# Kernel tuning notes

Hardware: AMD Instinct MI355X
Metric: run time of the kernel (lower is better)

## Reference

```python
import jax, jax.numpy as jnp
import numpy as np

L, B, N, D, H, DH, DFF = 12, 4, 512, 768, 12, 64, 3072
SCALE = 1.0 / np.sqrt(DH).astype(np.float32)


def _ln(x, s, b):
    m = x.mean(-1, keepdims=True)
    v = ((x - m) ** 2).mean(-1, keepdims=True)
    return (x - m) * jax.lax.rsqrt(v + 1e-5) * s + b


def setup_inputs() -> dict:
    key = jax.random.key(0)
    ks = jax.random.split(key, 6)
    w = 0.02
    return {
        "x": jax.random.normal(ks[0], (B, N, D), jnp.float32),
        "ln1_s": jnp.ones((L, D), jnp.float32),
        "ln1_b": jnp.zeros((L, D), jnp.float32),
        "wqkv": jax.random.normal(ks[1], (L, D, 3 * H * DH), jnp.float32) * w,
        "wo": jax.random.normal(ks[2], (L, H * DH, D), jnp.float32) * w,
        "bo": jnp.zeros((L, D), jnp.float32),
        "ln2_s": jnp.ones((L, D), jnp.float32),
        "ln2_b": jnp.zeros((L, D), jnp.float32),
        "w1": jax.random.normal(ks[3], (L, D, DFF), jnp.float32) * w,
        "b1": jnp.zeros((L, DFF), jnp.float32),
        "w2": jax.random.normal(ks[4], (L, DFF, D), jnp.float32) * w,
        "b2": jnp.zeros((L, D), jnp.float32),
    }


def reference(x, ln1_s, ln1_b, wqkv, wo, bo, ln2_s, ln2_b, w1, b1, w2, b2):
    b, n, d = x.shape

    def layer(x, p):
        l1s, l1b, qkv_w, wo_, bo_, l2s, l2b, w1_, b1_, w2_, b2_ = p
        # --- pre-norm multi-head self-attention (softmax) ---
        h = _ln(x, l1s, l1b)
        qkv = h @ qkv_w                              # [b, n, 3*H*DH]
        q, k, v = jnp.split(qkv, 3, axis=-1)
        def heads(t):                                # [b, n, H*DH] -> [b, H, n, DH]
            return t.reshape(b, n, H, DH).transpose(0, 2, 1, 3)
        q, k, v = heads(q), heads(k), heads(v)
        scores = jnp.einsum("bhnd,bhmd->bhnm", q, k) * SCALE
        attn = jax.nn.softmax(scores, axis=-1)       # [b, H, n, n]
        o = jnp.einsum("bhnm,bhmd->bhnd", attn, v)
        o = o.transpose(0, 2, 1, 3).reshape(b, n, H * DH)
        x = x + (o @ wo_ + bo_)                      # residual 1 (dropout p=0)
        # --- pre-norm feed-forward (GELU, exact erf as in torch) ---
        h2 = _ln(x, l2s, l2b)
        ff = jax.nn.gelu(h2 @ w1_ + b1_, approximate=False) @ w2_ + b2_
        x = x + ff                                   # residual 2
        return x, attn

    out, weights = jax.lax.scan(
        layer, x, (ln1_s, ln1_b, wqkv, wo, bo, ln2_s, ln2_b, w1, b1, w2, b2)
    )
    return out, weights  # weights: [L, b, H, n, n], matching the per-layer list
```

## Files before the change

kernel.cpp:

```cpp
#include <hip/hip_runtime.h>
#include <hip/hip_bf16.h>

typedef __hip_bfloat16 bf16;
typedef float f32x4 __attribute__((ext_vector_type(4)));
typedef __bf16 b16x8 __attribute__((ext_vector_type(8)));

constexpr int Lc = 12, Bc = 4, Nc = 512, Dc = 768, Hc = 12, DHc = 64, DFFc = 3072;
constexpr int QKVc = 3 * Dc;
constexpr int Mrows = Bc * Nc;
constexpr float SCALE = 0.125f;

__device__ __forceinline__ bf16 f2b(float x) { return __float2bfloat16(x); }

__device__ __forceinline__ void mfma_bf16(f32x4& d, b16x8 a, b16x8 b) {
  d = __builtin_amdgcn_mfma_f32_16x16x32_bf16(a, b, d, 0, 0, 0);
}

__device__ __forceinline__ void gload16(const bf16* g, bf16* l) {
  __builtin_amdgcn_global_load_lds(
      (const __attribute__((address_space(1))) void*)g,
      (__attribute__((address_space(3))) void*)l, 16, 0, 0);
}

template <int BM, int BN, int WM, int WN, int MODE, int SPLITK = 1>
__global__ __launch_bounds__(256) void gemm_bt(
    const bf16* __restrict__ Abase, const bf16* __restrict__ Btbase,
    const float* __restrict__ bias, float* __restrict__ xres,
    bf16* __restrict__ outb_,
    int M, int N, int K, int lda, int ldb, int ldc) {
  constexpr int MI = WM / 16, NI = WN / 16;
  constexpr int NWN = BN / WN;
  const int tid = threadIdx.x;
  const int lane = tid & 63, wave = tid >> 6;
  const int wm = (wave / NWN) * WM, wn = (wave % NWN) * WN;
  const int tm0 = blockIdx.x * BM, tn0 = blockIdx.y * BN;
  const int z = blockIdx.z;

  const bf16* A = Abase;
  const bf16* Bt = Btbase;
  bf16* outb = outb_;

  if (MODE == 4) {
    A = Abase + (size_t)z * Nc * Nc;
    Bt = Btbase + (size_t)z * DHc * Nc;
    outb = outb_ + (size_t)(z / Hc) * Nc * Dc + (size_t)(z % Hc) * DHc;
  }

  const int Kslice = K / SPLITK;
  const int kbase = (SPLITK > 1) ? z * Kslice : 0;

  __shared__ __align__(16) bf16 As[2][BM * 32];
  __shared__ __align__(16) bf16 Bs[2][BN * 32];

  f32x4 acc[MI][NI] = {};

  const int nt = Kslice >> 5;

  auto stage = [&](int buf, int k0) {
    #pragma unroll
    for (int rr = 0; rr < BM / 64; rr++) {
      int e = rr * 2048 + tid * 8;
      int r = e >> 5, kk = e & 31;
      gload16(A + (size_t)(tm0 + r) * lda + (kbase + k0 + kk), &As[buf][e]);
    }
    #pragma unroll
    for (int rr = 0; rr < BN / 64; rr++) {
      int e = rr * 2048 + tid * 8;
      int r = e >> 5, kk = e & 31;
      gload16(Bt + (size_t)(tn0 + r) * ldb + (kbase + k0 + kk), &Bs[buf][e]);
    }
  };

  stage(0, 0);
  __syncthreads();

  int cur = 0;
  for (int kt = 0; kt < nt; kt++) {
    if (kt + 1 < nt) stage(cur ^ 1, (kt + 1) * 32);

    b16x8 af[MI], bfr[NI];
    #pragma unroll
    for (int i = 0; i < MI; i++)
      af[i] = *(const b16x8*)(&As[cur][(wm + i * 16 + (lane & 15)) * 32 + (lane >> 4) * 8]);
    #pragma unroll
    for (int j = 0; j < NI; j++)
      bfr[j] = *(const b16x8*)(&Bs[cur][(wn + j * 16 + (lane & 15)) * 32 + (lane >> 4) * 8]);
    #pragma unroll
    for (int i = 0; i < MI; i++)
      #pragma unroll
      for (int j = 0; j < NI; j++)
        mfma_bf16(acc[i][j], af[i], bfr[j]);

    __syncthreads();
    cur ^= 1;
  }

  const int r0 = (lane >> 4) * 4;
  const int c0 = lane & 15;
  #pragma unroll
  for (int i = 0; i < MI; i++) {
    #pragma unroll
    for (int j = 0; j < NI; j++) {
      #pragma unroll
      for (int r = 0; r < 4; r++) {
        int row = tm0 + wm + i * 16 + r0 + r;
        int col = tn0 + wn + j * 16 + c0;
        float v = acc[i][j][r];
        if (MODE == 0) {
          outb[(size_t)row * ldc + col] = f2b(v);
        } else if (MODE == 1) {
          v += bias[col];
          float g = 0.5f * v * (1.0f + erff(v * 0.70710678118654752f));
          outb[(size_t)row * ldc + col] = f2b(g);
        } else if (MODE == 2) {
          if (SPLITK > 1) {
            if (z == 0) v += bias[col];
            atomicAdd(&xres[(size_t)row * ldc + col], v);
          } else {
            v += bias[col];
            xres[(size_t)row * ldc + col] += v;
          }
        } else {
          outb[(size_t)row * ldc + col] = f2b(v);
        }
      }
    }
  }
}

__global__ __launch_bounds__(256) void qksm_k(const bf16* __restrict__ qkv,
                                              float* __restrict__ attn_f,
                                              bf16* __restrict__ attn_b) {
  const int bh = blockIdx.y;
  const int b = bh / Hc, h = bh % Hc;
  const int n0 = blockIdx.x * 32;
  const int tid = threadIdx.x, lane = tid & 63, wave = tid >> 6;
  const int wn = wave * 128;

  constexpr int KP = 72;
  __shared__ __align__(16) bf16 Ks[512 * KP];
  __shared__ float red[32][4];

  const bf16* qbase = qkv + (size_t)b * Nc * QKVc + h * DHc;
  const bf16* kbase = qbase + Dc;

  for (int e = tid * 8; e < 512 * 64; e += 256 * 8) {
    int kv = e >> 6, c = e & 63;
    *(uint4*)(Ks + kv * KP + c) = *(const uint4*)(kbase + (size_t)kv * QKVc + c);
  }
  b16x8 qf[2][2];
  #pragma unroll
  for (int ks = 0; ks < 2; ks++)
    #pragma unroll
    for (int i = 0; i < 2; i++)
      qf[ks][i] = *(const b16x8*)(qbase +
          (size_t)(n0 + i * 16 + (lane & 15)) * QKVc + ks * 32 + (lane >> 4) * 8);
  __syncthreads();

  f32x4 acc[2][8] = {};
  #pragma unroll
  for (int ks = 0; ks < 2; ks++) {
    #pragma unroll
    for (int j = 0; j < 8; j++) {
      b16x8 kf = *(const b16x8*)(Ks + (wn + j * 16 + (lane & 15)) * KP +
                                 ks * 32 + (lane >> 4) * 8);
      #pragma unroll
      for (int i = 0; i < 2; i++)
        mfma_bf16(acc[i][j], qf[ks][i], kf);
    }
  }

  #pragma unroll
  for (int i = 0; i < 2; i++)
    #pragma unroll
    for (int j = 0; j < 8; j++)
      acc[i][j] *= SCALE;

  const int r0 = (lane >> 4) * 4, c0 = lane & 15;
  float rmax[2][4];
  #pragma unroll
  for (int i = 0; i < 2; i++)
    #pragma unroll
    for (int rr = 0; rr < 4; rr++) {
      float m = -1e30f;
      #pragma unroll
      for (int j = 0; j < 8; j++) m = fmaxf(m, acc[i][j][rr]);
      #pragma unroll
      for (int o = 1; o < 16; o <<= 1) m = fmaxf(m, __shfl_xor(m, o));
      rmax[i][rr] = m;
    }
  if (c0 == 0) {
    #pragma unroll
    for (int i = 0; i < 2; i++)
      #pragma unroll
      for (int rr = 0; rr < 4; rr++)
        red[i * 16 + r0 + rr][wave] = rmax[i][rr];
  }
  __syncthreads();
  #pragma unroll
  for (int i = 0; i < 2; i++)
    #pragma unroll
    for (int rr = 0; rr < 4; rr++) {
      int r = i * 16 + r0 + rr;
      rmax[i][rr] = fmaxf(fmaxf(red[r][0], red[r][1]), fmaxf(red[r][2], red[r][3]));
    }
  __syncthreads();

  float rsum[2][4];
  #pragma unroll
  for (int i = 0; i < 2; i++)
    #pragma unroll
    for (int rr = 0; rr < 4; rr++) {
      float s = 0.f;
      #pragma unroll
      for (int j = 0; j < 8; j++) {
        float e = expf(acc[i][j][rr] - rmax[i][rr]);
        acc[i][j][rr] = e;
        s += e;
      }
      #pragma unroll
      for (int o = 1; o < 16; o <<= 1) s += __shfl_xor(s, o);
      rsum[i][rr] = s;
    }
  if (c0 == 0) {
    #pragma unroll
    for (int i = 0; i < 2; i++)
      #pragma unroll
      for (int rr = 0; rr < 4; rr++)
        red[i * 16 + r0 + rr][wave] = rsum[i][rr];
  }
  __syncthreads();
  #pragma unroll
  for (int i = 0; i < 2; i++)
    #pragma unroll
    for (int rr = 0; rr < 4; rr++) {
      int r = i * 16 + r0 + rr;
      rsum[i][rr] = 1.0f / (red[r][0] + red[r][1] + red[r][2] + red[r][3]);
    }

  float* of = attn_f + (size_t)bh * Nc * Nc;
  bf16*  ob = attn_b + (size_t)bh * Nc * Nc;
  #pragma unroll
  for (int i = 0; i < 2; i++)
    #pragma unroll
    for (int j = 0; j < 8; j++)
      #pragma unroll
      for (int rr = 0; rr < 4; rr++) {
        int row = n0 + i * 16 + r0 + rr;
        int col = wn + j * 16 + c0;
        float p = acc[i][j][rr] * rsum[i][rr];
        of[(size_t)row * Nc + col] = p;
        ob[(size_t)row * Nc + col] = f2b(p);
      }
}

__global__ __launch_bounds__(256) void ln_k(const float* __restrict__ x,
                                            const float* __restrict__ s,
                                            const float* __restrict__ b,
                                            bf16* __restrict__ out) {
  const int row = blockIdx.x, tid = threadIdx.x;
  const float* xr = x + (size_t)row * Dc;
  float a0 = xr[tid], a1 = xr[tid + 256], a2 = xr[tid + 512];
  float sum = a0 + a1 + a2;
  float sq = a0 * a0 + a1 * a1 + a2 * a2;
  #pragma unroll
  for (int o = 32; o; o >>= 1) {
    sum += __shfl_down(sum, o);
    sq += __shfl_down(sq, o);
  }
  __shared__ float s1[4], s2[4];
  if ((tid & 63) == 0) { s1[tid >> 6] = sum; s2[tid >> 6] = sq; }
  __syncthreads();
  sum = s1[0] + s1[1] + s1[2] + s1[3];
  sq = s2[0] + s2[1] + s2[2] + s2[3];
  float m = sum * (1.0f / Dc);
  float var = sq * (1.0f / Dc) - m * m;
  float rs = rsqrtf(var + 1e-5f);
  bf16* orow = out + (size_t)row * Dc;
  orow[tid]       = f2b((a0 - m) * rs * s[tid]       + b[tid]);
  orow[tid + 256] = f2b((a1 - m) * rs * s[tid + 256] + b[tid + 256]);
  orow[tid + 512] = f2b((a2 - m) * rs * s[tid + 512] + b[tid + 512]);
}

__global__ __launch_bounds__(256) void twb_all_k(
    const float* __restrict__ wqkv_l, const float* __restrict__ wo_l,
    const float* __restrict__ w1_l, const float* __restrict__ w2_l,
    bf16* __restrict__ wTq, bf16* __restrict__ wTo,
    bf16* __restrict__ wT1, bf16* __restrict__ wT2) {
  int f = blockIdx.x;
  const float* in;
  bf16* outp;
  int K, Nw, n0, k0;
  if (f < 432)       { in = wqkv_l; outp = wTq; K = Dc;   Nw = QKVc; n0 = (f % 36) * 64; k0 = (f / 36) * 64; }
  else if (f < 576)  { f -= 432;  in = wo_l; outp = wTo; K = Dc;   Nw = Dc;   n0 = (f % 12) * 64; k0 = (f / 12) * 64; }
  else if (f < 1152) { f -= 576;  in = w1_l; outp = wT1; K = Dc;   Nw = DFFc; n0 = (f % 48) * 64; k0 = (f / 48) * 64; }
  else               { f -= 1152; in = w2_l; outp = wT2; K = DFFc; Nw = Dc;   n0 = (f % 12) * 64; k0 = (f / 12) * 64; }

  __shared__ bf16 t[64][65];
  const int tx = threadIdx.x & 63, ty = threadIdx.x >> 6;
  #pragma unroll
  for (int kk = ty; kk < 64; kk += 4)
    t[tx][kk] = f2b(in[(size_t)(k0 + kk) * Nw + n0 + tx]);
  __syncthreads();
  #pragma unroll
  for (int nn = ty; nn < 64; nn += 4)
    outp[(size_t)(n0 + nn) * K + k0 + tx] = t[nn][tx];
}

__global__ __launch_bounds__(256) void vtrans_k(const bf16* __restrict__ qkv,
                                                bf16* __restrict__ vt) {
  const int bh = blockIdx.z;
  const int b = bh / Hc, h = bh % Hc;
  const int n0 = blockIdx.x * 64;
  const bf16* src = qkv + (size_t)b * Nc * QKVc + 2 * Dc + h * DHc;
  __shared__ bf16 t[64][65];
  const int tx = threadIdx.x & 63, ty = threadIdx.x >> 6;
  #pragma unroll
  for (int nn = ty; nn < 64; nn += 4)
    t[tx][nn] = src[(size_t)(n0 + nn) * QKVc + tx];
  __syncthreads();
  bf16* dst = vt + (size_t)bh * DHc * Nc;
  #pragma unroll
  for (int dd = ty; dd < 64; dd += 4)
    dst[(size_t)dd * Nc + n0 + tx] = t[dd][tx];
}

extern "C" void kernel_launch(void* const* d_in, const int* in_sizes, int n_in,
                              void* d_out, int out_size, void* d_ws, size_t ws_size,
                              hipStream_t stream) {
  const float* x_in  = (const float*)d_in[0];
  const float* ln1_s = (const float*)d_in[1];
  const float* ln1_b = (const float*)d_in[2];
  const float* wqkv  = (const float*)d_in[3];
  const float* wo    = (const float*)d_in[4];
  const float* bo    = (const float*)d_in[5];
  const float* ln2_s = (const float*)d_in[6];
  const float* ln2_b = (const float*)d_in[7];
  const float* w1    = (const float*)d_in[8];
  const float* b1    = (const float*)d_in[9];
  const float* w2    = (const float*)d_in[10];
  const float* b2    = (const float*)d_in[11];
  float* out = (float*)d_out;

  char* ws = (char*)d_ws;
  float* x      = (float*)(ws + 0);
  bf16* h       = (bf16*)(ws + 6291456);
  bf16* qkv     = (bf16*)(ws + 9437184);
  bf16* o       = (bf16*)(ws + 18874368);
  bf16* ff      = (bf16*)(ws + 22020096);
  bf16* vt      = (bf16*)(ws + 34603008);
  bf16* wTq     = (bf16*)(ws + 37748736);
  bf16* wTo     = (bf16*)(ws + 41287680);
  bf16* wT1     = (bf16*)(ws + 42467328);
  bf16* wT2     = (bf16*)(ws + 47185920);
  bf16* attn_bf = (bf16*)(ws + 51904512);
  if (ws_size < (size_t)77070336) return;

  hipMemcpyAsync(x, x_in, (size_t)Mrows * Dc * sizeof(float),
                 hipMemcpyDeviceToDevice, stream);

  constexpr size_t ATTN_BASE = (size_t)Mrows * Dc;
  constexpr size_t ATTN_L = (size_t)Bc * Hc * Nc * Nc;

  for (int l = 0; l < Lc; l++) {
    float* attn_l = out + ATTN_BASE + (size_t)l * ATTN_L;

    twb_all_k<<<1728, 256, 0, stream>>>(
        wqkv + (size_t)l * Dc * QKVc, wo + (size_t)l * Dc * Dc,
        w1 + (size_t)l * Dc * DFFc, w2 + (size_t)l * DFFc * Dc,
        wTq, wTo, wT1, wT2);

    ln_k<<<Mrows, 256, 0, stream>>>(x, ln1_s + l * Dc, ln1_b + l * Dc, h);
    gemm_bt<128, 128, 64, 64, 0><<<dim3(Mrows / 128, QKVc / 128, 1), 256, 0, stream>>>(
        h, wTq, nullptr, nullptr, qkv, Mrows, QKVc, Dc, Dc, Dc, QKVc);
    vtrans_k<<<dim3(Nc / 64, 1, Bc * Hc), 256, 0, stream>>>(qkv, vt);
    qksm_k<<<dim3(Nc / 32, Bc * Hc), 256, 0, stream>>>(qkv, attn_l, attn_bf);
    gemm_bt<64, 64, 32, 32, 4><<<dim3(Nc / 64, 1, Bc * Hc), 256, 0, stream>>>(
        attn_bf, vt, nullptr, nullptr, o, Nc, DHc, Nc, Nc, Nc, Dc);
    gemm_bt<128, 64, 64, 32, 2, 2><<<dim3(Mrows / 128, Dc / 64, 2), 256, 0, stream>>>(
        o, wTo, bo + l * Dc, x, nullptr, Mrows, Dc, Dc, Dc, Dc, Dc);

    ln_k<<<Mrows, 256, 0, stream>>>(x, ln2_s + l * Dc, ln2_b + l * Dc, h);
    gemm_bt<128, 128, 64, 64, 1><<<dim3(Mrows / 128, DFFc / 128, 1), 256, 0, stream>>>(
        h, wT1, b1 + l * DFFc, nullptr, ff, Mrows, DFFc, Dc, Dc, Dc, DFFc);
    gemm_bt<128, 64, 64, 32, 2, 4><<<dim3(Mrows / 128, Dc / 64, 4), 256, 0, stream>>>(
        ff, wT2, b2 + l * Dc, x, nullptr, Mrows, Dc, DFFc, DFFc, DFFc, Dc);
  }

  hipMemcpyAsync(out, x, (size_t)Mrows * Dc * sizeof(float),
                 hipMemcpyDeviceToDevice, stream);
}
```

Before: 2.120 ms.

## Fuse P@V into the QK-softmax kernel via swizzled LDS probability tile

The separate attention-times-V GEMM is folded into the score/softmax kernel. Normalized probabilities go to a swizzled bf16 LDS tile, and the K buffer is reused to hold V^T so each block computes its 32x64 output slice directly. This removes the bf16 attention-matrix round trip through global memory (about 25 MB written and read per layer) and one kernel launch per layer. The cost is higher LDS use per block (about 104 KB), which may lower occupancy, plus extra register pressure from prefetching V into registers.

```diff
diff --git a/kernel.cpp b/kernel.cpp
--- a/kernel.cpp
+++ b/kernel.cpp
@@ -39,12 +39,6 @@
   const bf16* A = Abase;
   const bf16* Bt = Btbase;
   bf16* outb = outb_;
-
-  if (MODE == 4) {
-    A = Abase + (size_t)z * Nc * Nc;
-    Bt = Btbase + (size_t)z * DHc * Nc;
-    outb = outb_ + (size_t)(z / Hc) * Nc * Dc + (size_t)(z % Hc) * DHc;
-  }
 
   const int Kslice = K / SPLITK;
   const int kbase = (SPLITK > 1) ? z * Kslice : 0;
@@ -120,17 +114,16 @@
             v += bias[col];
             xres[(size_t)row * ldc + col] += v;
           }
-        } else {
-          outb[(size_t)row * ldc + col] = f2b(v);
         }
       }
     }
   }
 }
 
-__global__ __launch_bounds__(256) void qksm_k(const bf16* __restrict__ qkv,
-                                              float* __restrict__ attn_f,
-                                              bf16* __restrict__ attn_b) {
+__global__ __launch_bounds__(256) void fattn_k(const bf16* __restrict__ qkv,
+                                               const bf16* __restrict__ vt,
+                                               float* __restrict__ attn_f,
+                                               bf16* __restrict__ o) {
   const int bh = blockIdx.y;
   const int b = bh / Hc, h = bh % Hc;
   const int n0 = blockIdx.x * 32;
@@ -138,15 +131,16 @@
   const int wn = wave * 128;
 
   constexpr int KP = 72;
-  __shared__ __align__(16) bf16 Ks[512 * KP];
+  __shared__ __align__(16) bf16 KV[512 * KP];
+  __shared__ __align__(16) bf16 P[32 * 512];
   __shared__ float red[32][4];
 
   const bf16* qbase = qkv + (size_t)b * Nc * QKVc + h * DHc;
   const bf16* kbase = qbase + Dc;
 
-  for (int e = tid * 8; e < 512 * 64; e += 256 * 8) {
+  for (int e = tid * 8; e < 512 * 64; e += 2048) {
     int kv = e >> 6, c = e & 63;
-    *(uint4*)(Ks + kv * KP + c) = *(const uint4*)(kbase + (size_t)kv * QKVc + c);
+    *(uint4*)(KV + kv * KP + c) = *(const uint4*)(kbase + (size_t)kv * QKVc + c);
   }
   b16x8 qf[2][2];
   #pragma unroll
@@ -162,7 +156,7 @@
   for (int ks = 0; ks < 2; ks++) {
     #pragma unroll
     for (int j = 0; j < 8; j++) {
-      b16x8 kf = *(const b16x8*)(Ks + (wn + j * 16 + (lane & 15)) * KP +
+      b16x8 kf = *(const b16x8*)(KV + (wn + j * 16 + (lane & 15)) * KP +
                                  ks * 32 + (lane >> 4) * 8);
       #pragma unroll
       for (int i = 0; i < 2; i++)
@@ -170,6 +164,12 @@
     }
   }
 
+  const bf16* vthead = vt + (size_t)bh * DHc * Nc;
+  b16x8 vreg[16];
+  #pragma unroll
+  for (int r = 0; r < 16; r++)
+    vreg[r] = *(const b16x8*)(vthead + r * 2048 + tid * 8);
+
   #pragma unroll
   for (int i = 0; i < 2; i++)
     #pragma unroll
@@ -186,7 +186,7 @@
       #pragma unroll
       for (int j = 0; j < 8; j++) m = fmaxf(m, acc[i][j][rr]);
       #pragma unroll
-      for (int o = 1; o < 16; o <<= 1) m = fmaxf(m, __shfl_xor(m, o));
+      for (int of = 1; of < 16; of <<= 1) m = fmaxf(m, __shfl_xor(m, of));
       rmax[i][rr] = m;
     }
   if (c0 == 0) {
@@ -219,7 +219,7 @@
         s += e;
       }
       #pragma unroll
-      for (int o = 1; o < 16; o <<= 1) s += __shfl_xor(s, o);
+      for (int of = 1; of < 16; of <<= 1) s += __shfl_xor(s, of);
       rsum[i][rr] = s;
     }
   if (c0 == 0) {
@@ -238,20 +238,48 @@
       rsum[i][rr] = 1.0f / (red[r][0] + red[r][1] + red[r][2] + red[r][3]);
     }
 
-  float* of = attn_f + (size_t)bh * Nc * Nc;
-  bf16*  ob = attn_b + (size_t)bh * Nc * Nc;
+  #pragma unroll
+  for (int r = 0; r < 16; r++) {
+    int d = r * 4 + wave;
+    int kvs = (lane * 8) ^ ((d & 7) << 3);
+    *(uint4*)(KV + d * 512 + kvs) = *(uint4*)&vreg[r];
+  }
+
+  float* of32 = attn_f + (size_t)bh * Nc * Nc;
   #pragma unroll
   for (int i = 0; i < 2; i++)
     #pragma unroll
     for (int j = 0; j < 8; j++)
       #pragma unroll
       for (int rr = 0; rr < 4; rr++) {
-        int row = n0 + i * 16 + r0 + rr;
+        int rloc = i * 16 + r0 + rr;
         int col = wn + j * 16 + c0;
         float p = acc[i][j][rr] * rsum[i][rr];
-        of[(size_t)row * Nc + col] = p;
-        ob[(size_t)row * Nc + col] = f2b(p);
+        of32[(size_t)(n0 + rloc) * Nc + col] = p;
+        P[rloc * 512 + (col ^ ((rloc & 7) << 3))] = f2b(p);
       }
+  __syncthreads();
+
+  f32x4 oacc[2] = {};
+  #pragma unroll
+  for (int ks = 0; ks < 16; ks++) {
+    int kvb = ks * 32 + ((lane >> 4) << 3);
+    int dd = wave * 16 + (lane & 15);
+    b16x8 bf_ = *(const b16x8*)(KV + dd * 512 + (kvb ^ ((dd & 7) << 3)));
+    #pragma unroll
+    for (int i = 0; i < 2; i++) {
+      int q = i * 16 + (lane & 15);
+      b16x8 af_ = *(const b16x8*)(P + q * 512 + (kvb ^ ((q & 7) << 3)));
+      mfma_bf16(oacc[i], af_, bf_);
+    }
+  }
+  #pragma unroll
+  for (int i = 0; i < 2; i++)
+    #pragma unroll
+    for (int r = 0; r < 4; r++) {
+      int row = b * Nc + n0 + i * 16 + r0 + r;
+      o[(size_t)row * Dc + h * DHc + wave * 16 + c0] = f2b(oacc[i][r]);
+    }
 }
 
 __global__ __launch_bounds__(256) void ln_k(const float* __restrict__ x,
@@ -353,8 +381,7 @@
   bf16* wTo     = (bf16*)(ws + 41287680);
   bf16* wT1     = (bf16*)(ws + 42467328);
   bf16* wT2     = (bf16*)(ws + 47185920);
-  bf16* attn_bf = (bf16*)(ws + 51904512);
-  if (ws_size < (size_t)77070336) return;
+  if (ws_size < (size_t)51904512) return;
 
   hipMemcpyAsync(x, x_in, (size_t)Mrows * Dc * sizeof(float),
                  hipMemcpyDeviceToDevice, stream);
@@ -374,9 +401,7 @@
     gemm_bt<128, 128, 64, 64, 0><<<dim3(Mrows / 128, QKVc / 128, 1), 256, 0, stream>>>(
         h, wTq, nullptr, nullptr, qkv, Mrows, QKVc, Dc, Dc, Dc, QKVc);
     vtrans_k<<<dim3(Nc / 64, 1, Bc * Hc), 256, 0, stream>>>(qkv, vt);
-    qksm_k<<<dim3(Nc / 32, Bc * Hc), 256, 0, stream>>>(qkv, attn_l, attn_bf);
-    gemm_bt<64, 64, 32, 32, 4><<<dim3(Nc / 64, 1, Bc * Hc), 256, 0, stream>>>(
-        attn_bf, vt, nullptr, nullptr, o, Nc, DHc, Nc, Nc, Nc, Dc);
+    fattn_k<<<dim3(Nc / 32, Bc * Hc), 256, 0, stream>>>(qkv, vt, attn_l, o);
     gemm_bt<128, 64, 64, 32, 2, 2><<<dim3(Mrows / 128, Dc / 64, 2), 256, 0, stream>>>(
         o, wTo, bo + l * Dc, x, nullptr, Mrows, Dc, Dc, Dc, Dc, Dc);
 
```

Result: no change. 2.138 ms (+0.8%).
